# Kernel tuning notes

Measured on AMD Instinct MI355X. Metric: run time of the kernel, lower is better.

The kernel has to match this reference:

```python
import jax, jax.numpy as jnp
import numpy as np
from functools import partial

B, N_BINS, T = 64, 64, 256
N_FILTERS = 64
H = 512
RNN_IN = N_FILTERS * (N_BINS - 2)  # conv with 3x3 kernel, pad (0,1): height -> n_bins-2


def setup_inputs() -> dict:
    key = jax.random.key(0)
    ks = jax.random.split(key, 20)
    s = 1.0 / np.sqrt(H)
    inp = {
        'x': jax.random.normal(ks[0], (B, 1, N_BINS, T), jnp.float32),
        'h1': jnp.zeros((B, H), jnp.float32),
        'h2': jnp.zeros((B, H), jnp.float32),
        'h3': jnp.zeros((B, H), jnp.float32),
        'conv_w': jax.random.normal(ks[1], (N_FILTERS, 1, 3, 3), jnp.float32) * 0.1,
        'conv_b': jax.random.normal(ks[2], (N_FILTERS,), jnp.float32) * 0.1,
    }
    in_sizes = [RNN_IN, H, H]
    for l in range(3):
        k = 3 + 4 * l
        inp[f'w_ih{l}'] = jax.random.normal(ks[k], (3 * H, in_sizes[l]), jnp.float32) * s
        inp[f'w_hh{l}'] = jax.random.normal(ks[k + 1], (3 * H, H), jnp.float32) * s
        inp[f'b_ih{l}'] = jax.random.normal(ks[k + 2], (3 * H,), jnp.float32) * s
        inp[f'b_hh{l}'] = jax.random.normal(ks[k + 3], (3 * H,), jnp.float32) * s
    return inp


def gru_cell(x, h, w_ih, w_hh, b_ih, b_hh):
    # PyTorch GRUCell: gates ordered (r, z, n); r multiplies (W_hn h + b_hn)
    gi = x @ w_ih.T + b_ih  # [B, 3H]
    gh = h @ w_hh.T + b_hh  # [B, 3H]
    i_r, i_z, i_n = jnp.split(gi, 3, axis=-1)
    h_r, h_z, h_n = jnp.split(gh, 3, axis=-1)
    r = jax.nn.sigmoid(i_r + h_r)
    z = jax.nn.sigmoid(i_z + h_z)
    n = jnp.tanh(i_n + r * h_n)
    return (1.0 - z) * n + z * h


def reference(x, h1, h2, h3, conv_w, conv_b,
              w_ih0, w_hh0, b_ih0, b_hh0,
              w_ih1, w_hh1, b_ih1, b_hh1,
              w_ih2, w_hh2, b_ih2, b_hh2):
    # Conv2d(1, n_filters, (3,3), stride=1, padding=(0,1)): [B,1,Nb,T] -> [B,F,Nb-2,T]
    y = jax.lax.conv_general_dilated(
        x, conv_w, window_strides=(1, 1), padding=[(0, 0), (1, 1)],
        dimension_numbers=('NCHW', 'OIHW', 'NCHW'))
    y = y + conv_b[None, :, None, None]
    b, t = x.shape[0], x.shape[3]
    y = y.reshape(b, RNN_IN, t)              # collapse (F, H_out) -> rnn_in_size
    xs = jnp.transpose(y, (2, 0, 1))         # [T, B, rnn_in]

    def step(carry, xt):
        c1, c2, c3 = carry
        c1 = gru_cell(xt, c1, w_ih0, w_hh0, b_ih0, b_hh0)
        c2 = gru_cell(c1, c2, w_ih1, w_hh1, b_ih1, b_hh1)
        c3 = gru_cell(c2, c3, w_ih2, w_hh2, b_ih2, b_hh2)
        return (c1, c2, c3), c3

    _, out = jax.lax.scan(step, (h1, h2, h3), xs)
    return out  # [T, B, H]
```

## Files before the change

kernel.cpp:

```cpp
#include <hip/hip_runtime.h>
#include <hip/hip_fp16.h>

#define BATCH 64
#define TLEN  256
#define HD    512
#define G3    1536
#define KIN0  192
#define XT_S  258
#define XT_STRIDE (XT_S*64)
#define NBLOCKS 96
#define NKS_HH 16
#define NKS_I0 6
#define HS (BATCH*HD)

typedef _Float16 f16;
typedef unsigned long long u64;
typedef __attribute__((ext_vector_type(8))) _Float16 half8;
typedef __attribute__((ext_vector_type(4))) float    f32x4;

__device__ __forceinline__ f32x4 mfma16(half8 a, half8 b, f32x4 c) {
    return __builtin_amdgcn_mfma_f32_16x16x32_f16(a, b, c, 0, 0, 0);
}

#define LD16(dst, base, OFF)                                                  \
    asm volatile("global_load_dwordx4 %0, %1, off offset:" #OFF " sc0 sc1"    \
                 : "=v"(dst) : "v"(base))

#define LDALL16(arr, base) do {                                               \
    LD16(arr[0],  base, 0);   LD16(arr[1],  base, 64);                        \
    LD16(arr[2],  base, 128); LD16(arr[3],  base, 192);                       \
    LD16(arr[4],  base, 256); LD16(arr[5],  base, 320);                       \
    LD16(arr[6],  base, 384); LD16(arr[7],  base, 448);                       \
    LD16(arr[8],  base, 512); LD16(arr[9],  base, 576);                       \
    LD16(arr[10], base, 640); LD16(arr[11], base, 704);                       \
    LD16(arr[12], base, 768); LD16(arr[13], base, 832);                       \
    LD16(arr[14], base, 896); LD16(arr[15], base, 960);                       \
} while (0)

#define WAIT_VM0()                                         \
    do {                                                   \
        asm volatile("s_waitcnt vmcnt(0)" ::: "memory");   \
        __builtin_amdgcn_sched_barrier(0);                 \
    } while (0)

#define FLAGP(flags, l, s, w) ((flags) + ((((l) * 32 + (s)) * 4 + (w)) * 16))


__global__ void fold_w3(const float* __restrict__ wih0,
                        const float* __restrict__ convw,
                        f16* __restrict__ w3) {
    int idx = blockIdx.x * 256 + threadIdx.x;
    if (idx >= G3 * KIN0) return;
    int g  = idx / KIN0;
    int kk = idx % KIN0;
    int dt = kk >> 6;
    int i  = kk & 63;
    float s = 0.f;
    for (int dr = 0; dr < 3; ++dr) {
        int r = i - dr;
        if (r < 0 || r >= 62) continue;
        const float* wrow = wih0 + (size_t)g * 3968 + r;
        #pragma unroll 8
        for (int f = 0; f < 64; ++f)
            s += wrow[f * 62] * convw[f * 9 + dr * 3 + dt];
    }
    w3[(size_t)g * KIN0 + kk] = (f16)s;
}

__global__ void fold_bias0(const float* __restrict__ wih0,
                           const float* __restrict__ convb,
                           const float* __restrict__ bih0,
                           float* __restrict__ bias0) {
    int w    = (blockIdx.x * 256 + threadIdx.x) >> 6;
    int lane = threadIdx.x & 63;
    if (w >= G3) return;
    const float* wrow = wih0 + (size_t)w * 3968;
    float s = 0.f;
    for (int e = lane; e < 3968; e += 64) s += wrow[e] * convb[e / 62];
    #pragma unroll
    for (int o = 32; o > 0; o >>= 1) s += __shfl_down(s, o);
    if (lane == 0) bias0[w] = s + bih0[w];
}

struct Ptr5 { const float* p[5]; };

__global__ void cvt_weights(Ptr5 src, f16* __restrict__ dst) {
    int idx = blockIdx.x * 256 + threadIdx.x;
    if (idx >= 5 * G3 * HD) return;
    int m = idx / (G3 * HD), off = idx % (G3 * HD);
    dst[idx] = (f16)src.p[m][off];
}

__global__ void build_xt(const float* __restrict__ x, f16* __restrict__ xt) {
    int idx = blockIdx.x * 256 + threadIdx.x;
    if (idx >= BATCH * XT_S * 64) return;
    int b = idx / (XT_S * 64);
    int rem = idx % (XT_S * 64);
    int s = rem / 64, i = rem & 63;
    float v = 0.f;
    if (s >= 1 && s <= 256) v = x[(size_t)b * (64 * TLEN) + (size_t)i * TLEN + (s - 1)];
    xt[idx] = (f16)v;
}

__global__ void init_h(const float* __restrict__ h1, const float* __restrict__ h2,
                       const float* __restrict__ h3, f16* __restrict__ hbuf,
                       unsigned* __restrict__ flags) {
    int idx = blockIdx.x * 256 + threadIdx.x;
    if (idx < 6144) flags[idx] = 0u;
    if (idx >= HS) return;
    hbuf[1 * HS + idx] = (f16)h1[idx];
    hbuf[3 * HS + idx] = (f16)h2[idx];
    hbuf[5 * HS + idx] = (f16)h3[idx];
}


__global__ __launch_bounds__(256, 1) void gru_persistent(
    const f16* __restrict__ xT, const f16* __restrict__ W3,
    const f16* __restrict__ wts,
    const float* __restrict__ bias0, const float* __restrict__ bhh0,
    const float* __restrict__ bih1,  const float* __restrict__ bhh1,
    const float* __restrict__ bih2,  const float* __restrict__ bhh2,
    f16* __restrict__ hb, float* __restrict__ out, unsigned* __restrict__ flags)
{
    __shared__ f16 wih_lds[3 * NKS_HH * 64 * 8];
    __shared__ f16 whh_lds[3 * NKS_HH * 64 * 8];

    const int bid   = blockIdx.x;
    const int layer = bid >> 5;
    const int slice = bid & 31;
    const int j0    = slice * 16;
    const int tid   = threadIdx.x;
    const int lane  = tid & 63;
    const int wid   = tid >> 6;
    const int b0    = wid * 16;
    const int jc    = lane & 15;
    const int kg    = lane >> 4;
    const int j     = j0 + jc;

    const int KIN  = (layer == 0) ? KIN0 : HD;
    const int nksI = (layer == 0) ? NKS_I0 : NKS_HH;
    const f16* wih_g = (layer == 0) ? W3 : (wts + (size_t)(2 * layer - 1) * (G3 * HD));
    const f16* whh_g = wts + (size_t)(2 * layer) * (G3 * HD);

    for (int e = tid; e < 3 * nksI * 64; e += 256) {
        int le = e & 63;
        int ks = (e >> 6) % nksI;
        int g  = (e >> 6) / nksI;
        int row = j0 + (le & 15);
        int col = ks * 32 + (le >> 4) * 8;
        *(half8*)&wih_lds[(size_t)e * 8] =
            *(const half8*)(wih_g + (size_t)(g * HD + row) * KIN + col);
    }
    for (int e = tid; e < 3 * NKS_HH * 64; e += 256) {
        int le = e & 63;
        int ks = (e >> 6) % NKS_HH;
        int g  = (e >> 6) / NKS_HH;
        int row = j0 + (le & 15);
        int col = ks * 32 + (le >> 4) * 8;
        *(half8*)&whh_lds[(size_t)e * 8] =
            *(const half8*)(whh_g + (size_t)(g * HD + row) * HD + col);
    }

    const float* bih = (layer == 0) ? bias0 : ((layer == 1) ? bih1 : bih2);
    const float* bhh = (layer == 0) ? bhh0  : ((layer == 1) ? bhh1 : bhh2);
    const float bRs = bih[j] + bhh[j];
    const float bZs = bih[HD + j] + bhh[HD + j];
    const float bin = bih[2 * HD + j];
    const float bhn = bhh[2 * HD + j];

    f16* hbase = hb + (size_t)layer * 2 * HS;
    const f16* xprev = (layer == 0) ? nullptr : (hb + (size_t)(layer - 1) * 2 * HS);

    float hpr[4];
    {
        const f16* hinit = hbase + 1 * HS;
        #pragma unroll
        for (int rr = 0; rr < 4; ++rr)
            hpr[rr] = (float)hinit[(size_t)(b0 + kg * 4 + rr) * HD + j];
    }

    __syncthreads();

    const f16* fW = wih_lds + lane * 8;
    const f16* fH = whh_lds + lane * 8;

    const unsigned* pMain;  int mainOff;
    if (layer == 0) {
        pMain = (lane < 32) ? FLAGP(flags, 0, lane, wid) : nullptr;
        mainOff = 0;
    } else if (lane < 32) {
        pMain = FLAGP(flags, layer - 1, lane, wid);
        mainOff = 1;
    } else {
        pMain = FLAGP(flags, layer, lane - 32, wid);
        mainOff = 0;
    }
    const unsigned* pAnti = (layer < 2 && lane < 32)
                          ? FLAGP(flags, layer + 1, lane, wid) : nullptr;
    unsigned* pMine = FLAGP(flags, layer, slice, wid);

    for (int R = 0; R < XT_S; ++R) {
        const int t = R - layer;
        const bool active = (t >= 0) && (t < TLEN);
        if (!active) continue;

        f32x4 aRx = {0.f,0.f,0.f,0.f}, aZx = {0.f,0.f,0.f,0.f}, aNi = {0.f,0.f,0.f,0.f};
        f32x4 aRh = {0.f,0.f,0.f,0.f}, aZh = {0.f,0.f,0.f,0.f}, aNh = {0.f,0.f,0.f,0.f};

        if (layer == 0) {
            const f16* xb = xT + (size_t)(b0 + jc) * XT_STRIDE + (size_t)t * 64 + kg * 8;
            #pragma unroll
            for (int ks = 0; ks < NKS_I0; ++ks) {
                half8 a = *(const half8*)(xb + ks * 32);
                aRx = mfma16(a, *(const half8*)(fW + (0 * NKS_I0 + ks) * 512), aRx);
                aZx = mfma16(a, *(const half8*)(fW + (1 * NKS_I0 + ks) * 512), aZx);
                aNi = mfma16(a, *(const half8*)(fW + (2 * NKS_I0 + ks) * 512), aNi);
            }
        }

        {
            bool pend = (pMain != nullptr);
            const unsigned req = (unsigned)(t + mainOff);
            while (__any(pend)) {
                if (pend)
                    pend = __hip_atomic_load(pMain, __ATOMIC_RELAXED,
                                             __HIP_MEMORY_SCOPE_AGENT) < req;
            }
            asm volatile("" ::: "memory");
        }

        const f16* hold = hbase + ((t - 1) & 1) * HS;
        const f16* hbp  = hold + (size_t)(b0 + jc) * HD + kg * 8;
        half8 ah[NKS_HH];
        LDALL16(ah, hbp);

        half8 ax[NKS_HH];
        if (layer > 0) {
            const f16* xbp = xprev + (t & 1) * HS + (size_t)(b0 + jc) * HD + kg * 8;
            LDALL16(ax, xbp);
        }

        if (layer < 2 && t >= 2) {
            bool pend = (pAnti != nullptr);
            const unsigned req = (unsigned)(t - 1);
            while (__any(pend)) {
                if (pend)
                    pend = __hip_atomic_load(pAnti, __ATOMIC_RELAXED,
                                             __HIP_MEMORY_SCOPE_AGENT) < req;
            }
            asm volatile("" ::: "memory");
        }

        WAIT_VM0();

        if (layer > 0) {
            #pragma unroll
            for (int ks = 0; ks < NKS_HH; ++ks) {
                aRx = mfma16(ax[ks], *(const half8*)(fW + (0 * NKS_HH + ks) * 512), aRx);
                aZx = mfma16(ax[ks], *(const half8*)(fW + (1 * NKS_HH + ks) * 512), aZx);
                aNi = mfma16(ax[ks], *(const half8*)(fW + (2 * NKS_HH + ks) * 512), aNi);
                aRh = mfma16(ah[ks], *(const half8*)(fH + (0 * NKS_HH + ks) * 512), aRh);
                aZh = mfma16(ah[ks], *(const half8*)(fH + (1 * NKS_HH + ks) * 512), aZh);
                aNh = mfma16(ah[ks], *(const half8*)(fH + (2 * NKS_HH + ks) * 512), aNh);
            }
        } else {
            #pragma unroll
            for (int ks = 0; ks < NKS_HH; ++ks) {
                aRh = mfma16(ah[ks], *(const half8*)(fH + (0 * NKS_HH + ks) * 512), aRh);
                aZh = mfma16(ah[ks], *(const half8*)(fH + (1 * NKS_HH + ks) * 512), aZh);
                aNh = mfma16(ah[ks], *(const half8*)(fH + (2 * NKS_HH + ks) * 512), aNh);
            }
        }

        float hv[4];
        #pragma unroll
        for (int rr = 0; rr < 4; ++rr) {
            float r = 1.f / (1.f + __expf(-(aRx[rr] + aRh[rr] + bRs)));
            float z = 1.f / (1.f + __expf(-(aZx[rr] + aZh[rr] + bZs)));
            float nv = aNi[rr] + bin + r * (aNh[rr] + bhn);
            float e  = __expf(2.f * nv);
            float n  = 1.f - 2.f / (e + 1.f);
            hv[rr] = (1.f - z) * n + z * hpr[rr];
            hpr[rr] = hv[rr];
        }

        f16* hnew = hbase + (t & 1) * HS;
        #pragma unroll
        for (int rr = 0; rr < 4; ++rr) {
            int brow = b0 + kg * 4 + rr;
            float nbv = __shfl_xor(hv[rr], 1);
            unsigned short ua = __builtin_bit_cast(unsigned short, (f16)hv[rr]);
            unsigned short ub = __builtin_bit_cast(unsigned short, (f16)nbv);
            unsigned pk = (unsigned)ua | ((unsigned)ub << 16);
            unsigned pk2 = __shfl_xor(pk, 2);
            if ((jc & 3) == 0) {
                u64 val = (u64)pk | ((u64)pk2 << 32);
                (void)__hip_atomic_exchange((u64*)(hnew + (size_t)brow * HD + j), val,
                                            __ATOMIC_RELAXED, __HIP_MEMORY_SCOPE_AGENT);
            }
        }

        WAIT_VM0();
        if (lane == 0)
            (void)__hip_atomic_exchange(pMine, (unsigned)(t + 1),
                                        __ATOMIC_RELAXED, __HIP_MEMORY_SCOPE_AGENT);

        if (layer == 2) {
            #pragma unroll
            for (int rr = 0; rr < 4; ++rr) {
                int brow = b0 + kg * 4 + rr;
                out[(size_t)t * HS + (size_t)brow * HD + j] = hv[rr];
            }
        }
    }
}


extern "C" void kernel_launch(void* const* d_in, const int* in_sizes, int n_in,
                              void* d_out, int out_size, void* d_ws, size_t ws_size,
                              hipStream_t stream) {
    const float* x     = (const float*)d_in[0];
    const float* h1    = (const float*)d_in[1];
    const float* h2    = (const float*)d_in[2];
    const float* h3    = (const float*)d_in[3];
    const float* convw = (const float*)d_in[4];
    const float* convb = (const float*)d_in[5];
    const float* wih0  = (const float*)d_in[6];
    const float* whh0  = (const float*)d_in[7];
    const float* bih0  = (const float*)d_in[8];
    const float* bhh0  = (const float*)d_in[9];
    const float* wih1  = (const float*)d_in[10];
    const float* whh1  = (const float*)d_in[11];
    const float* bih1  = (const float*)d_in[12];
    const float* bhh1  = (const float*)d_in[13];
    const float* wih2  = (const float*)d_in[14];
    const float* whh2  = (const float*)d_in[15];
    const float* bih2  = (const float*)d_in[16];
    const float* bhh2  = (const float*)d_in[17];

    char* ws = (char*)d_ws;
    unsigned* flags = (unsigned*)(ws + 0);
    f16*   W3    = (f16*)(ws + 24576);
    float* bias0 = (float*)(ws + 614400);
    f16*   wts   = (f16*)(ws + 620544);
    f16*   xT    = (f16*)(ws + 8484864);
    f16*   hb    = (f16*)(ws + 10598400);

    fold_w3   <<<(G3 * KIN0 + 255) / 256, 256, 0, stream>>>(wih0, convw, W3);
    fold_bias0<<<(G3 * 64 + 255) / 256,   256, 0, stream>>>(wih0, convb, bih0, bias0);
    Ptr5 p5; p5.p[0] = whh0; p5.p[1] = wih1; p5.p[2] = whh1; p5.p[3] = wih2; p5.p[4] = whh2;
    cvt_weights<<<(5 * G3 * HD + 255) / 256, 256, 0, stream>>>(p5, wts);
    build_xt  <<<(BATCH * XT_S * 64 + 255) / 256, 256, 0, stream>>>(x, xT);
    init_h    <<<(HS + 255) / 256, 256, 0, stream>>>(h1, h2, h3, hb, flags);

    gru_persistent<<<NBLOCKS, 256, 0, stream>>>(
        xT, W3, wts, bias0, bhh0, bih1, bhh1, bih2, bhh2,
        hb, (float*)d_out, flags);
}
```

Baseline: 1.991 ms.

## Use counter-based sub-group flags and a 4-deep hidden-state ring buffer

Replaces per-slice flag polling (32 flags per wave) with fetch-add counters aggregated over 8 slices each, so each wave polls only 4 counters. The hidden-state double buffer becomes a 4-slot ring, which relaxes the anti-dependency wait on the next layer to lag by 4 steps. The input-projection MFMAs for layers 1-2 are now issued before waiting on the same layer's previous hidden state, overlapping them with that wait. The cost is atomic contention on the shared counters and a larger workspace for the hidden states.

```diff
diff --git a/kernel.cpp b/kernel.cpp
--- a/kernel.cpp
+++ b/kernel.cpp
@@ -12,6 +12,7 @@
 #define NKS_HH 16
 #define NKS_I0 6
 #define HS (BATCH*HD)
+#define RING 4
 
 typedef _Float16 f16;
 typedef unsigned long long u64;
@@ -43,7 +44,7 @@
         __builtin_amdgcn_sched_barrier(0);                 \
     } while (0)
 
-#define FLAGP(flags, l, s, w) ((flags) + ((((l) * 32 + (s)) * 4 + (w)) * 16))
+#define SUBP(flags, l, w, g) ((flags) + ((((l) * 4 + (w)) * 4 + (g)) * 16))
 
 
 __global__ void fold_w3(const float* __restrict__ wih0,
@@ -106,11 +107,11 @@
                        const float* __restrict__ h3, f16* __restrict__ hbuf,
                        unsigned* __restrict__ flags) {
     int idx = blockIdx.x * 256 + threadIdx.x;
-    if (idx < 6144) flags[idx] = 0u;
+    if (idx < 1024) flags[idx] = 0u;
     if (idx >= HS) return;
-    hbuf[1 * HS + idx] = (f16)h1[idx];
-    hbuf[3 * HS + idx] = (f16)h2[idx];
-    hbuf[5 * HS + idx] = (f16)h3[idx];
+    hbuf[(0 * RING + 3) * (size_t)HS + idx] = (f16)h1[idx];
+    hbuf[(1 * RING + 3) * (size_t)HS + idx] = (f16)h2[idx];
+    hbuf[(2 * RING + 3) * (size_t)HS + idx] = (f16)h3[idx];
 }
 
 
@@ -168,12 +169,12 @@
     const float bin = bih[2 * HD + j];
     const float bhn = bhh[2 * HD + j];
 
-    f16* hbase = hb + (size_t)layer * 2 * HS;
-    const f16* xprev = (layer == 0) ? nullptr : (hb + (size_t)(layer - 1) * 2 * HS);
+    f16* hbase = hb + (size_t)layer * RING * HS;
+    const f16* xprev = (layer == 0) ? nullptr : (hb + (size_t)(layer - 1) * RING * HS);
 
     float hpr[4];
     {
-        const f16* hinit = hbase + 1 * HS;
+        const f16* hinit = hbase + 3 * (size_t)HS;
         #pragma unroll
         for (int rr = 0; rr < 4; ++rr)
             hpr[rr] = (float)hinit[(size_t)(b0 + kg * 4 + rr) * HD + j];
@@ -184,25 +185,16 @@
     const f16* fW = wih_lds + lane * 8;
     const f16* fH = whh_lds + lane * 8;
 
-    const unsigned* pMain;  int mainOff;
-    if (layer == 0) {
-        pMain = (lane < 32) ? FLAGP(flags, 0, lane, wid) : nullptr;
-        mainOff = 0;
-    } else if (lane < 32) {
-        pMain = FLAGP(flags, layer - 1, lane, wid);
-        mainOff = 1;
-    } else {
-        pMain = FLAGP(flags, layer, lane - 32, wid);
-        mainOff = 0;
-    }
-    const unsigned* pAnti = (layer < 2 && lane < 32)
-                          ? FLAGP(flags, layer + 1, lane, wid) : nullptr;
-    unsigned* pMine = FLAGP(flags, layer, slice, wid);
+    const unsigned* pX    = (layer > 0 && lane < 4)
+                          ? SUBP(flags, layer - 1, wid, lane) : nullptr;
+    const unsigned* pAnti = (layer < 2 && lane >= 4 && lane < 8)
+                          ? SUBP(flags, layer + 1, wid, lane - 4) : nullptr;
+    const unsigned* pOwn  = (lane < 4) ? SUBP(flags, layer, wid, lane) : nullptr;
+    unsigned* pAdd = SUBP(flags, layer, wid, slice & 3);
 
     for (int R = 0; R < XT_S; ++R) {
         const int t = R - layer;
-        const bool active = (t >= 0) && (t < TLEN);
-        if (!active) continue;
+        if (t < 0 || t >= TLEN) continue;
 
         f32x4 aRx = {0.f,0.f,0.f,0.f}, aZx = {0.f,0.f,0.f,0.f}, aNi = {0.f,0.f,0.f,0.f};
         f32x4 aRh = {0.f,0.f,0.f,0.f}, aZh = {0.f,0.f,0.f,0.f}, aNh = {0.f,0.f,0.f,0.f};
@@ -219,51 +211,51 @@
         }
 
         {
-            bool pend = (pMain != nullptr);
-            const unsigned req = (unsigned)(t + mainOff);
+            bool pend; unsigned req;
+            if (lane < 4)      { pend = (pX != nullptr);
+                                 req  = 8u * (unsigned)(t + 1); }
+            else if (lane < 8) { pend = (pAnti != nullptr) && (t >= 4);
+                                 req  = 8u * (unsigned)(t - 3); }
+            else               { pend = false; req = 0; }
+            const unsigned* p = (lane < 4) ? pX : pAnti;
             while (__any(pend)) {
                 if (pend)
-                    pend = __hip_atomic_load(pMain, __ATOMIC_RELAXED,
+                    pend = __hip_atomic_load(p, __ATOMIC_RELAXED,
                                              __HIP_MEMORY_SCOPE_AGENT) < req;
             }
             asm volatile("" ::: "memory");
         }
 
-        const f16* hold = hbase + ((t - 1) & 1) * HS;
-        const f16* hbp  = hold + (size_t)(b0 + jc) * HD + kg * 8;
-        half8 ah[NKS_HH];
-        LDALL16(ah, hbp);
-
-        half8 ax[NKS_HH];
         if (layer > 0) {
-            const f16* xbp = xprev + (t & 1) * HS + (size_t)(b0 + jc) * HD + kg * 8;
+            const f16* xbp = xprev + (size_t)(t & 3) * HS + (size_t)(b0 + jc) * HD + kg * 8;
+            half8 ax[NKS_HH];
             LDALL16(ax, xbp);
-        }
-
-        if (layer < 2 && t >= 2) {
-            bool pend = (pAnti != nullptr);
-            const unsigned req = (unsigned)(t - 1);
-            while (__any(pend)) {
-                if (pend)
-                    pend = __hip_atomic_load(pAnti, __ATOMIC_RELAXED,
-                                             __HIP_MEMORY_SCOPE_AGENT) < req;
-            }
-            asm volatile("" ::: "memory");
-        }
-
-        WAIT_VM0();
-
-        if (layer > 0) {
+            WAIT_VM0();
             #pragma unroll
             for (int ks = 0; ks < NKS_HH; ++ks) {
                 aRx = mfma16(ax[ks], *(const half8*)(fW + (0 * NKS_HH + ks) * 512), aRx);
                 aZx = mfma16(ax[ks], *(const half8*)(fW + (1 * NKS_HH + ks) * 512), aZx);
                 aNi = mfma16(ax[ks], *(const half8*)(fW + (2 * NKS_HH + ks) * 512), aNi);
-                aRh = mfma16(ah[ks], *(const half8*)(fH + (0 * NKS_HH + ks) * 512), aRh);
-                aZh = mfma16(ah[ks], *(const half8*)(fH + (1 * NKS_HH + ks) * 512), aZh);
-                aNh = mfma16(ah[ks], *(const half8*)(fH + (2 * NKS_HH + ks) * 512), aNh);
-            }
-        } else {
+            }
+        }
+
+        {
+            bool pend = (pOwn != nullptr) && (t > 0);
+            const unsigned req = 8u * (unsigned)t;
+            while (__any(pend)) {
+                if (pend)
+                    pend = __hip_atomic_load(pOwn, __ATOMIC_RELAXED,
+                                             __HIP_MEMORY_SCOPE_AGENT) < req;
+            }
+            asm volatile("" ::: "memory");
+        }
+
+        {
+            const f16* hbp = hbase + (size_t)((t - 1) & 3) * HS
+                           + (size_t)(b0 + jc) * HD + kg * 8;
+            half8 ah[NKS_HH];
+            LDALL16(ah, hbp);
+            WAIT_VM0();
             #pragma unroll
             for (int ks = 0; ks < NKS_HH; ++ks) {
                 aRh = mfma16(ah[ks], *(const half8*)(fH + (0 * NKS_HH + ks) * 512), aRh);
@@ -284,7 +276,7 @@
             hpr[rr] = hv[rr];
         }
 
-        f16* hnew = hbase + (t & 1) * HS;
+        f16* hnew = hbase + (size_t)(t & 3) * HS;
         #pragma unroll
         for (int rr = 0; rr < 4; ++rr) {
             int brow = b0 + kg * 4 + rr;
@@ -302,8 +294,8 @@
 
         WAIT_VM0();
         if (lane == 0)
-            (void)__hip_atomic_exchange(pMine, (unsigned)(t + 1),
-                                        __ATOMIC_RELAXED, __HIP_MEMORY_SCOPE_AGENT);
+            (void)__hip_atomic_fetch_add(pAdd, 1u, __ATOMIC_RELAXED,
+                                         __HIP_MEMORY_SCOPE_AGENT);
 
         if (layer == 2) {
             #pragma unroll
@@ -340,11 +332,11 @@
 
     char* ws = (char*)d_ws;
     unsigned* flags = (unsigned*)(ws + 0);
-    f16*   W3    = (f16*)(ws + 24576);
-    float* bias0 = (float*)(ws + 614400);
-    f16*   wts   = (f16*)(ws + 620544);
-    f16*   xT    = (f16*)(ws + 8484864);
-    f16*   hb    = (f16*)(ws + 10598400);
+    f16*   W3    = (f16*)(ws + 4096);
+    float* bias0 = (float*)(ws + 593920);
+    f16*   wts   = (f16*)(ws + 600064);
+    f16*   xT    = (f16*)(ws + 8464384);
+    f16*   hb    = (f16*)(ws + 10577920);
 
     fold_w3   <<<(G3 * KIN0 + 255) / 256, 256, 0, stream>>>(wih0, convw, W3);
     fold_bias0<<<(G3 * 64 + 255) / 256,   256, 0, stream>>>(wih0, convb, bih0, bias0);
```

Result: faster. 1.605 ms (median of 2 runs) (-19.4%).
